# Performance work log

Measured on AMD Instinct MI355X. Metric: run time of the kernel, lower is better.

Reference implementation:

```python
import jax, jax.numpy as jnp
import numpy as np

THRESHOLD = 1.0
SLOPE = 25.0  # snntorch surrogate.fast_sigmoid default

@jax.custom_vjp
def spike_fn(x):
    # heaviside forward, fast_sigmoid surrogate backward
    return (x > 0).astype(x.dtype)

def _spike_fwd(x):
    return spike_fn(x), x

def _spike_bwd(x, g):
    return (g / (SLOPE * jnp.abs(x) + 1.0) ** 2,)

spike_fn.defvjp(_spike_fwd, _spike_bwd)


def setup_inputs() -> dict:
    key = jax.random.key(0)
    ks = jax.random.split(key, 8)
    B, D_IN, H0, H1 = 16384, 512, 1024, 512
    def linear_params(kw, kb, fan_in, fan_out):
        bound = 1.0 / np.sqrt(fan_in)
        w = jax.random.uniform(kw, (fan_out, fan_in), jnp.float32, -bound, bound)
        b = jax.random.uniform(kb, (fan_out,), jnp.float32, -bound, bound)
        return w, b
    w1, b1 = linear_params(ks[0], ks[1], D_IN, H0)
    w2, b2 = linear_params(ks[2], ks[3], H0, H1)
    w3, b3 = linear_params(ks[4], ks[5], H1, 1)
    data = jax.random.normal(ks[6], (B, D_IN), jnp.float32)
    return {"data": data, "w1": w1, "b1": b1, "w2": w2, "b2": b2,
            "w3": w3, "b3": b3, "time_steps": 8}


def reference(data, w1, b1, w2, b2, w3, b3, time_steps):
    # Effective betas: snntorch clamps beta to [0,1]. lif1 beta = units0 (=1024) -> 1.0 (source bug, replicated).
    beta1 = jnp.float32(1.0)
    beta2 = jnp.float32(0.95)
    # data is constant across time, so fc1 output is step-invariant
    cur1 = data @ w1.T + b1                      # [B, H0]
    B, H0 = cur1.shape
    H1 = w2.shape[0]
    mem1_0 = jnp.zeros((B, H0), cur1.dtype)
    mem2_0 = jnp.zeros((B, H1), cur1.dtype)

    def step(carry, _):
        mem1, mem2 = carry
        # snntorch Leaky (reset_mechanism='subtract'): reset detected on OLD mem, detached
        reset1 = jax.lax.stop_gradient((mem1 > THRESHOLD).astype(mem1.dtype))
        mem1 = beta1 * mem1 + cur1 - reset1 * THRESHOLD
        spk1 = spike_fn(mem1 - THRESHOLD)
        cur2 = spk1 @ w2.T + b2                  # [B, H1]
        reset2 = jax.lax.stop_gradient((mem2 > THRESHOLD).astype(mem2.dtype))
        mem2 = beta2 * mem2 + cur2 - reset2 * THRESHOLD
        spk2 = spike_fn(mem2 - THRESHOLD)
        cur3 = spk2 @ w3.T + b3                  # [B, 1]
        return (mem1, mem2), cur3

    _, cur3_seq = jax.lax.scan(step, (mem1_0, mem2_0), None, length=time_steps)
    return jnp.mean(cur3_seq, axis=0)            # [B, 1]
```

## Files before the change

kernel.cpp:

```cpp
#include <hip/hip_runtime.h>
#include <hip/hip_bf16.h>
#include <cstdint>
#include <cstddef>


#define NB 16384
#define DIN 512
#define NH0 1024
#define NH1 512

typedef float f32x4 __attribute__((ext_vector_type(4)));
typedef short bf16x8 __attribute__((ext_vector_type(8)));

__global__ void init_out_kernel(float* __restrict__ out,
                                const float* __restrict__ b3, int n) {
    int i = blockIdx.x * blockDim.x + threadIdx.x;
    if (i < n) out[i] = b3[0];
}

__global__ __launch_bounds__(256) void gemm1_spike_kernel(
    const float* __restrict__ data, const float* __restrict__ w1,
    const float* __restrict__ b1, uint8_t* __restrict__ pat)
{
    __shared__ float As[64][68];
    __shared__ float Bs[64][68];
    const int tid = threadIdx.x;
    const int tx = tid & 15, ty = tid >> 4;
    const int i0 = blockIdx.x * 64, n0 = blockIdx.y * 64;

    float acc[4][4] = {};

    for (int kb = 0; kb < DIN; kb += 64) {
        #pragma unroll
        for (int rep = 0; rep < 4; ++rep) {
            int idx = tid + rep * 256;
            int row = idx >> 4, c4 = (idx & 15) * 4;
            float4 va = *(const float4*)(data + (size_t)(i0 + row) * DIN + kb + c4);
            *(float4*)(&As[row][c4]) = va;
            float4 vb = *(const float4*)(w1 + (size_t)(n0 + row) * DIN + kb + c4);
            *(float4*)(&Bs[row][c4]) = vb;
        }
        __syncthreads();
        #pragma unroll 4
        for (int k4 = 0; k4 < 16; ++k4) {
            float4 a4[4], b4[4];
            #pragma unroll
            for (int ii = 0; ii < 4; ++ii)
                a4[ii] = *(const float4*)(&As[ty + ii * 16][k4 * 4]);
            #pragma unroll
            for (int nn = 0; nn < 4; ++nn)
                b4[nn] = *(const float4*)(&Bs[tx + nn * 16][k4 * 4]);
            #pragma unroll
            for (int ii = 0; ii < 4; ++ii) {
                #pragma unroll
                for (int nn = 0; nn < 4; ++nn) {
                    acc[ii][nn] = fmaf(a4[ii].x, b4[nn].x, acc[ii][nn]);
                    acc[ii][nn] = fmaf(a4[ii].y, b4[nn].y, acc[ii][nn]);
                    acc[ii][nn] = fmaf(a4[ii].z, b4[nn].z, acc[ii][nn]);
                    acc[ii][nn] = fmaf(a4[ii].w, b4[nn].w, acc[ii][nn]);
                }
            }
        }
        __syncthreads();
    }

    #pragma unroll
    for (int ii = 0; ii < 4; ++ii) {
        int i = i0 + ty + ii * 16;
        #pragma unroll
        for (int nn = 0; nn < 4; ++nn) {
            int n = n0 + tx + nn * 16;
            float x = __fadd_rn(acc[ii][nn], b1[n]);
            float mem = 0.0f;
            unsigned p = 0;
            #pragma unroll
            for (int t = 0; t < 8; ++t) {
                bool reset = mem > 1.0f;
                float tmp = __fadd_rn(mem, x);
                mem = reset ? __fsub_rn(tmp, 1.0f) : tmp;
                p |= (mem > 1.0f ? 1u : 0u) << t;
            }
            pat[(size_t)i * NH0 + n] = (uint8_t)p;
        }
    }
}

__device__ inline uint16_t f2bf(float f) {
    __hip_bfloat16 h = __float2bfloat16(f);
    return *reinterpret_cast<uint16_t*>(&h);
}
__device__ inline float bf2f(uint16_t u) {
    __hip_bfloat16 h = *reinterpret_cast<__hip_bfloat16*>(&u);
    return __bfloat162float(h);
}

__global__ __launch_bounds__(256, 2) void gemm2_mfma_kernel(
    const uint8_t* __restrict__ pat, const float* __restrict__ w2,
    const float* __restrict__ b2, const float* __restrict__ w3,
    float* __restrict__ out)
{
    __shared__ __align__(16) uint16_t Bhi[64][72];
    __shared__ __align__(16) uint16_t Bmd[64][72];
    __shared__ __align__(16) uint16_t Blo[64][72];
    __shared__ __align__(16) uint8_t  Ap[64][80];

    const int tid  = threadIdx.x;
    const int lane = tid & 63;
    const int wv   = tid >> 6;
    const int lr   = lane & 15;
    const int lg   = lane >> 4;
    const int i0   = blockIdx.x * 64, n0 = blockIdx.y * 64;

    f32x4 acc[8][4];
    #pragma unroll
    for (int t = 0; t < 8; ++t)
        #pragma unroll
        for (int nf = 0; nf < 4; ++nf)
            acc[t][nf] = (f32x4)(0.0f);

    const int srow = tid >> 2;
    const int scol = (tid & 3) * 16;

    for (int kb = 0; kb < NH0; kb += 64) {
        __syncthreads();
        const float* wsrc = w2 + (size_t)(n0 + srow) * NH0 + kb + scol;
        #pragma unroll
        for (int g = 0; g < 2; ++g) {
            float4 f0 = *(const float4*)(wsrc + g * 8);
            float4 f1 = *(const float4*)(wsrc + g * 8 + 4);
            float f[8] = {f0.x, f0.y, f0.z, f0.w, f1.x, f1.y, f1.z, f1.w};
            uint32_t hw[4], mw[4], lw[4];
            #pragma unroll
            for (int e = 0; e < 4; ++e) {
                float a = f[2 * e], b = f[2 * e + 1];
                uint16_t h0 = f2bf(a), h1 = f2bf(b);
                float d0 = __fsub_rn(a, bf2f(h0));
                float d1 = __fsub_rn(b, bf2f(h1));
                uint16_t m0 = f2bf(d0), m1 = f2bf(d1);
                float e0 = __fsub_rn(d0, bf2f(m0));
                float e1 = __fsub_rn(d1, bf2f(m1));
                uint16_t l0 = f2bf(e0), l1 = f2bf(e1);
                hw[e] = (uint32_t)h0 | ((uint32_t)h1 << 16);
                mw[e] = (uint32_t)m0 | ((uint32_t)m1 << 16);
                lw[e] = (uint32_t)l0 | ((uint32_t)l1 << 16);
            }
            *(uint4*)(&Bhi[srow][scol + g * 8]) = make_uint4(hw[0], hw[1], hw[2], hw[3]);
            *(uint4*)(&Bmd[srow][scol + g * 8]) = make_uint4(mw[0], mw[1], mw[2], mw[3]);
            *(uint4*)(&Blo[srow][scol + g * 8]) = make_uint4(lw[0], lw[1], lw[2], lw[3]);
        }
        {
            uint4 pv = *(const uint4*)(pat + (size_t)(i0 + srow) * NH0 + kb + scol);
            *(uint4*)(&Ap[srow][scol]) = pv;
        }
        __syncthreads();

        #pragma unroll
        for (int s = 0; s < 2; ++s) {
            const int k0 = s * 32;
            bf16x8 bh[4], bm[4], bl[4];
            #pragma unroll
            for (int nf = 0; nf < 4; ++nf) {
                const int col = nf * 16 + lr;
                bh[nf] = *(const bf16x8*)(&Bhi[col][k0 + lg * 8]);
                bm[nf] = *(const bf16x8*)(&Bmd[col][k0 + lg * 8]);
                bl[nf] = *(const bf16x8*)(&Blo[col][k0 + lg * 8]);
            }
            const uint2 p8 = *(const uint2*)(&Ap[wv * 16 + lr][k0 + lg * 8]);
            #pragma unroll
            for (int t = 0; t < 8; ++t) {
                uint32_t y0 = (p8.x >> t) & 0x01010101u;
                uint32_t y1 = (p8.y >> t) & 0x01010101u;
                uint32_t s0 = __builtin_amdgcn_perm(0u, y0, 0x01010000u) | 0x02000200u;
                uint32_t s1 = __builtin_amdgcn_perm(0u, y0, 0x03030202u) | 0x02000200u;
                uint32_t s2 = __builtin_amdgcn_perm(0u, y1, 0x01010000u) | 0x02000200u;
                uint32_t s3 = __builtin_amdgcn_perm(0u, y1, 0x03030202u) | 0x02000200u;
                union { uint4 u; bf16x8 v; } af;
                af.u = make_uint4(__builtin_amdgcn_perm(0u, 0x3F008000u, s0),
                                  __builtin_amdgcn_perm(0u, 0x3F008000u, s1),
                                  __builtin_amdgcn_perm(0u, 0x3F008000u, s2),
                                  __builtin_amdgcn_perm(0u, 0x3F008000u, s3));
                #pragma unroll
                for (int nf = 0; nf < 4; ++nf) {
                    acc[t][nf] = __builtin_amdgcn_mfma_f32_16x16x32_bf16(
                        af.v, bh[nf], acc[t][nf], 0, 0, 0);
                    acc[t][nf] = __builtin_amdgcn_mfma_f32_16x16x32_bf16(
                        af.v, bm[nf], acc[t][nf], 0, 0, 0);
                    acc[t][nf] = __builtin_amdgcn_mfma_f32_16x16x32_bf16(
                        af.v, bl[nf], acc[t][nf], 0, 0, 0);
                }
            }
        }
    }

    float rowsum[4] = {0.0f, 0.0f, 0.0f, 0.0f};
    #pragma unroll
    for (int nf = 0; nf < 4; ++nf) {
        const int n = n0 + nf * 16 + lr;
        const float b2n = b2[n];
        const float w3n = w3[n];
        #pragma unroll
        for (int r = 0; r < 4; ++r) {
            float mem = 0.0f;
            int pc = 0;
            #pragma unroll
            for (int t = 0; t < 8; ++t) {
                bool reset = mem > 1.0f;
                float x   = __fadd_rn(acc[t][nf][r], b2n);
                float tmp = __fadd_rn(__fmul_rn(0.95f, mem), x);
                mem = reset ? __fsub_rn(tmp, 1.0f) : tmp;
                pc += (mem > 1.0f) ? 1 : 0;
            }
            rowsum[r] = fmaf(w3n, (float)pc, rowsum[r]);
        }
    }
    #pragma unroll
    for (int r = 0; r < 4; ++r) {
        float s = rowsum[r];
        s += __shfl_xor(s, 1);
        s += __shfl_xor(s, 2);
        s += __shfl_xor(s, 4);
        s += __shfl_xor(s, 8);
        if (lr == 0)
            atomicAdd(&out[i0 + wv * 16 + lg * 4 + r], 0.125f * s);
    }
}

extern "C" void kernel_launch(void* const* d_in, const int* in_sizes, int n_in,
                              void* d_out, int out_size, void* d_ws, size_t ws_size,
                              hipStream_t stream) {
    const float* data = (const float*)d_in[0];
    const float* w1   = (const float*)d_in[1];
    const float* b1   = (const float*)d_in[2];
    const float* w2   = (const float*)d_in[3];
    const float* b2   = (const float*)d_in[4];
    const float* w3   = (const float*)d_in[5];
    const float* b3   = (const float*)d_in[6];
    float* out = (float*)d_out;
    uint8_t* pat = (uint8_t*)d_ws;

    init_out_kernel<<<(NB + 255) / 256, 256, 0, stream>>>(out, b3, NB);
    gemm1_spike_kernel<<<dim3(NB / 64, NH0 / 64), 256, 0, stream>>>(data, w1, b1, pat);
    gemm2_mfma_kernel<<<dim3(NB / 64, NH1 / 64), 256, 0, stream>>>(pat, w2, b2, w3, out);
}
```

Measured before the change: 607.2 us.

## Pre-split w2 into bf16 triples once, enlarge gemm1 tile, read spikes directly

Adds a small kernel that splits w2 into hi/mid/lo bf16 arrays in the workspace once per call, so every gemm2 block loads pre-split weights instead of redoing the conversion per tile. gemm1 now computes 128x64 tiles (8x4 per thread) with an occupancy hint of 3, which improves reuse of w1 tiles. gemm2 also drops its LDS staging of the spike pattern and reads pattern bytes straight from global memory per lane. The trade-offs are extra workspace traffic for the split weights, higher register pressure in gemm1, and uncoalesced global pattern loads.

After: 623.1 us. +2.6%, slower.

```diff
diff --git a/kernel.cpp b/kernel.cpp
--- a/kernel.cpp
+++ b/kernel.cpp
@@ -12,46 +12,96 @@
 typedef float f32x4 __attribute__((ext_vector_type(4)));
 typedef short bf16x8 __attribute__((ext_vector_type(8)));
 
+#define WS_PAT   0u
+#define WS_W2H   19922944u
+#define WS_W2M   20971520u
+#define WS_W2L   22020096u
+
+__device__ inline uint16_t f2bf(float f) {
+    __hip_bfloat16 h = __float2bfloat16(f);
+    return *reinterpret_cast<uint16_t*>(&h);
+}
+__device__ inline float bf2f(uint16_t u) {
+    __hip_bfloat16 h = *reinterpret_cast<__hip_bfloat16*>(&u);
+    return __bfloat162float(h);
+}
+
 __global__ void init_out_kernel(float* __restrict__ out,
                                 const float* __restrict__ b3, int n) {
     int i = blockIdx.x * blockDim.x + threadIdx.x;
     if (i < n) out[i] = b3[0];
 }
 
-__global__ __launch_bounds__(256) void gemm1_spike_kernel(
+__global__ __launch_bounds__(256) void split3_kernel(
+    const float* __restrict__ src, uint16_t* __restrict__ h,
+    uint16_t* __restrict__ m, uint16_t* __restrict__ l, int n)
+{
+    int i = (blockIdx.x * 256 + threadIdx.x) * 4;
+    if (i >= n) return;
+    float4 f = *(const float4*)(src + i);
+    float fv[4] = {f.x, f.y, f.z, f.w};
+    uint32_t hw[2], mw[2], lw[2];
+    #pragma unroll
+    for (int g = 0; g < 2; ++g) {
+        uint16_t hh[2], mm[2], ll[2];
+        #pragma unroll
+        for (int e = 0; e < 2; ++e) {
+            float a = fv[2 * g + e];
+            uint16_t h0 = f2bf(a);
+            float d = __fsub_rn(a, bf2f(h0));
+            uint16_t m0 = f2bf(d);
+            float e2 = __fsub_rn(d, bf2f(m0));
+            uint16_t l0 = f2bf(e2);
+            hh[e] = h0; mm[e] = m0; ll[e] = l0;
+        }
+        hw[g] = (uint32_t)hh[0] | ((uint32_t)hh[1] << 16);
+        mw[g] = (uint32_t)mm[0] | ((uint32_t)mm[1] << 16);
+        lw[g] = (uint32_t)ll[0] | ((uint32_t)ll[1] << 16);
+    }
+    *(uint2*)(h + i) = make_uint2(hw[0], hw[1]);
+    *(uint2*)(m + i) = make_uint2(mw[0], mw[1]);
+    *(uint2*)(l + i) = make_uint2(lw[0], lw[1]);
+}
+
+__global__ __launch_bounds__(256, 3) void gemm1_spike_kernel(
     const float* __restrict__ data, const float* __restrict__ w1,
     const float* __restrict__ b1, uint8_t* __restrict__ pat)
 {
-    __shared__ float As[64][68];
+    __shared__ float As[128][68];
     __shared__ float Bs[64][68];
     const int tid = threadIdx.x;
     const int tx = tid & 15, ty = tid >> 4;
-    const int i0 = blockIdx.x * 64, n0 = blockIdx.y * 64;
-
-    float acc[4][4] = {};
+    const int i0 = blockIdx.x * 128, n0 = blockIdx.y * 64;
+
+    float acc[8][4] = {};
 
     for (int kb = 0; kb < DIN; kb += 64) {
         #pragma unroll
-        for (int rep = 0; rep < 4; ++rep) {
+        for (int rep = 0; rep < 8; ++rep) {
             int idx = tid + rep * 256;
             int row = idx >> 4, c4 = (idx & 15) * 4;
             float4 va = *(const float4*)(data + (size_t)(i0 + row) * DIN + kb + c4);
             *(float4*)(&As[row][c4]) = va;
+        }
+        #pragma unroll
+        for (int rep = 0; rep < 4; ++rep) {
+            int idx = tid + rep * 256;
+            int row = idx >> 4, c4 = (idx & 15) * 4;
             float4 vb = *(const float4*)(w1 + (size_t)(n0 + row) * DIN + kb + c4);
             *(float4*)(&Bs[row][c4]) = vb;
         }
         __syncthreads();
         #pragma unroll 4
         for (int k4 = 0; k4 < 16; ++k4) {
-            float4 a4[4], b4[4];
-            #pragma unroll
-            for (int ii = 0; ii < 4; ++ii)
+            float4 a4[8], b4[4];
+            #pragma unroll
+            for (int ii = 0; ii < 8; ++ii)
                 a4[ii] = *(const float4*)(&As[ty + ii * 16][k4 * 4]);
             #pragma unroll
             for (int nn = 0; nn < 4; ++nn)
                 b4[nn] = *(const float4*)(&Bs[tx + nn * 16][k4 * 4]);
             #pragma unroll
-            for (int ii = 0; ii < 4; ++ii) {
+            for (int ii = 0; ii < 8; ++ii) {
                 #pragma unroll
                 for (int nn = 0; nn < 4; ++nn) {
                     acc[ii][nn] = fmaf(a4[ii].x, b4[nn].x, acc[ii][nn]);
@@ -65,7 +115,7 @@
     }
 
     #pragma unroll
-    for (int ii = 0; ii < 4; ++ii) {
+    for (int ii = 0; ii < 8; ++ii) {
         int i = i0 + ty + ii * 16;
         #pragma unroll
         for (int nn = 0; nn < 4; ++nn) {
@@ -85,24 +135,16 @@
     }
 }
 
-__device__ inline uint16_t f2bf(float f) {
-    __hip_bfloat16 h = __float2bfloat16(f);
-    return *reinterpret_cast<uint16_t*>(&h);
-}
-__device__ inline float bf2f(uint16_t u) {
-    __hip_bfloat16 h = *reinterpret_cast<__hip_bfloat16*>(&u);
-    return __bfloat162float(h);
-}
-
 __global__ __launch_bounds__(256, 2) void gemm2_mfma_kernel(
-    const uint8_t* __restrict__ pat, const float* __restrict__ w2,
+    const uint8_t* __restrict__ pat,
+    const uint16_t* __restrict__ w2h, const uint16_t* __restrict__ w2m,
+    const uint16_t* __restrict__ w2l,
     const float* __restrict__ b2, const float* __restrict__ w3,
     float* __restrict__ out)
 {
     __shared__ __align__(16) uint16_t Bhi[64][72];
     __shared__ __align__(16) uint16_t Bmd[64][72];
     __shared__ __align__(16) uint16_t Blo[64][72];
-    __shared__ __align__(16) uint8_t  Ap[64][80];
 
     const int tid  = threadIdx.x;
     const int lane = tid & 63;
@@ -120,38 +162,19 @@
 
     const int srow = tid >> 2;
     const int scol = (tid & 3) * 16;
+    const uint8_t* prow = pat + (size_t)(i0 + wv * 16 + lr) * NH0;
 
     for (int kb = 0; kb < NH0; kb += 64) {
         __syncthreads();
-        const float* wsrc = w2 + (size_t)(n0 + srow) * NH0 + kb + scol;
-        #pragma unroll
-        for (int g = 0; g < 2; ++g) {
-            float4 f0 = *(const float4*)(wsrc + g * 8);
-            float4 f1 = *(const float4*)(wsrc + g * 8 + 4);
-            float f[8] = {f0.x, f0.y, f0.z, f0.w, f1.x, f1.y, f1.z, f1.w};
-            uint32_t hw[4], mw[4], lw[4];
-            #pragma unroll
-            for (int e = 0; e < 4; ++e) {
-                float a = f[2 * e], b = f[2 * e + 1];
-                uint16_t h0 = f2bf(a), h1 = f2bf(b);
-                float d0 = __fsub_rn(a, bf2f(h0));
-                float d1 = __fsub_rn(b, bf2f(h1));
-                uint16_t m0 = f2bf(d0), m1 = f2bf(d1);
-                float e0 = __fsub_rn(d0, bf2f(m0));
-                float e1 = __fsub_rn(d1, bf2f(m1));
-                uint16_t l0 = f2bf(e0), l1 = f2bf(e1);
-                hw[e] = (uint32_t)h0 | ((uint32_t)h1 << 16);
-                mw[e] = (uint32_t)m0 | ((uint32_t)m1 << 16);
-                lw[e] = (uint32_t)l0 | ((uint32_t)l1 << 16);
-            }
-            *(uint4*)(&Bhi[srow][scol + g * 8]) = make_uint4(hw[0], hw[1], hw[2], hw[3]);
-            *(uint4*)(&Bmd[srow][scol + g * 8]) = make_uint4(mw[0], mw[1], mw[2], mw[3]);
-            *(uint4*)(&Blo[srow][scol + g * 8]) = make_uint4(lw[0], lw[1], lw[2], lw[3]);
-        }
-        {
-            uint4 pv = *(const uint4*)(pat + (size_t)(i0 + srow) * NH0 + kb + scol);
-            *(uint4*)(&Ap[srow][scol]) = pv;
-        }
+        const uint16_t* s1 = w2h + (size_t)(n0 + srow) * NH0 + kb + scol;
+        const uint16_t* s2 = w2m + (size_t)(n0 + srow) * NH0 + kb + scol;
+        const uint16_t* s3 = w2l + (size_t)(n0 + srow) * NH0 + kb + scol;
+        *(uint4*)(&Bhi[srow][scol])     = *(const uint4*)(s1);
+        *(uint4*)(&Bhi[srow][scol + 8]) = *(const uint4*)(s1 + 8);
+        *(uint4*)(&Bmd[srow][scol])     = *(const uint4*)(s2);
+        *(uint4*)(&Bmd[srow][scol + 8]) = *(const uint4*)(s2 + 8);
+        *(uint4*)(&Blo[srow][scol])     = *(const uint4*)(s3);
+        *(uint4*)(&Blo[srow][scol + 8]) = *(const uint4*)(s3 + 8);
         __syncthreads();
 
         #pragma unroll
@@ -165,20 +188,20 @@
                 bm[nf] = *(const bf16x8*)(&Bmd[col][k0 + lg * 8]);
                 bl[nf] = *(const bf16x8*)(&Blo[col][k0 + lg * 8]);
             }
-            const uint2 p8 = *(const uint2*)(&Ap[wv * 16 + lr][k0 + lg * 8]);
+            const uint2 p8 = *(const uint2*)(prow + kb + k0 + lg * 8);
             #pragma unroll
             for (int t = 0; t < 8; ++t) {
                 uint32_t y0 = (p8.x >> t) & 0x01010101u;
                 uint32_t y1 = (p8.y >> t) & 0x01010101u;
                 uint32_t s0 = __builtin_amdgcn_perm(0u, y0, 0x01010000u) | 0x02000200u;
-                uint32_t s1 = __builtin_amdgcn_perm(0u, y0, 0x03030202u) | 0x02000200u;
-                uint32_t s2 = __builtin_amdgcn_perm(0u, y1, 0x01010000u) | 0x02000200u;
-                uint32_t s3 = __builtin_amdgcn_perm(0u, y1, 0x03030202u) | 0x02000200u;
+                uint32_t s1x = __builtin_amdgcn_perm(0u, y0, 0x03030202u) | 0x02000200u;
+                uint32_t s2x = __builtin_amdgcn_perm(0u, y1, 0x01010000u) | 0x02000200u;
+                uint32_t s3x = __builtin_amdgcn_perm(0u, y1, 0x03030202u) | 0x02000200u;
                 union { uint4 u; bf16x8 v; } af;
                 af.u = make_uint4(__builtin_amdgcn_perm(0u, 0x3F008000u, s0),
-                                  __builtin_amdgcn_perm(0u, 0x3F008000u, s1),
-                                  __builtin_amdgcn_perm(0u, 0x3F008000u, s2),
-                                  __builtin_amdgcn_perm(0u, 0x3F008000u, s3));
+                                  __builtin_amdgcn_perm(0u, 0x3F008000u, s1x),
+                                  __builtin_amdgcn_perm(0u, 0x3F008000u, s2x),
+                                  __builtin_amdgcn_perm(0u, 0x3F008000u, s3x));
                 #pragma unroll
                 for (int nf = 0; nf < 4; ++nf) {
                     acc[t][nf] = __builtin_amdgcn_mfma_f32_16x16x32_bf16(
@@ -236,9 +259,15 @@
     const float* w3   = (const float*)d_in[5];
     const float* b3   = (const float*)d_in[6];
     float* out = (float*)d_out;
-    uint8_t* pat = (uint8_t*)d_ws;
+
+    char* ws = (char*)d_ws;
+    uint8_t*  pat = (uint8_t*)(ws + WS_PAT);
+    uint16_t* w2h = (uint16_t*)(ws + WS_W2H);
+    uint16_t* w2m = (uint16_t*)(ws + WS_W2M);
+    uint16_t* w2l = (uint16_t*)(ws + WS_W2L);
 
     init_out_kernel<<<(NB + 255) / 256, 256, 0, stream>>>(out, b3, NB);
-    gemm1_spike_kernel<<<dim3(NB / 64, NH0 / 64), 256, 0, stream>>>(data, w1, b1, pat);
-    gemm2_mfma_kernel<<<dim3(NB / 64, NH1 / 64), 256, 0, stream>>>(pat, w2, b2, w3, out);
-}
+    split3_kernel<<<(NH1 * NH0 / 4 + 255) / 256, 256, 0, stream>>>(w2, w2h, w2m, w2l, NH1 * NH0);
+    gemm1_spike_kernel<<<dim3(NB / 128, NH0 / 64), 256, 0, stream>>>(data, w1, b1, pat);
+    gemm2_mfma_kernel<<<dim3(NB / 64, NH1 / 64), 256, 0, stream>>>(pat, w2h, w2m, w2l, b2, w3, out);
+}
```
